# Kernel optimization log

Hardware: AMD Instinct MI355X
Metric: run time of the kernel (lower is better)

## Reference

```python
import jax, jax.numpy as jnp
import numpy as np

N, C = 800000, 80
B0, D0, H0, W0 = 4, 1, 360, 360


def setup_inputs() -> dict:
    key = jax.random.key(0)
    k1, k2, k3, k4, k5 = jax.random.split(key, 5)
    feats = jax.random.normal(k1, (N, C), dtype=jnp.float32)
    # coords columns: (x<W, y<H, z<D, b<B) -- per-column ranges so both rank
    # and flat geom index stay in-bounds, as in real LSS voxel coords.
    c0 = jax.random.randint(k2, (N,), 0, W0, dtype=jnp.int32)
    c1 = jax.random.randint(k3, (N,), 0, H0, dtype=jnp.int32)
    c2 = jax.random.randint(k4, (N,), 0, D0, dtype=jnp.int32)
    c3 = jax.random.randint(k5, (N,), 0, B0, dtype=jnp.int32)
    coords = jnp.stack([c0, c1, c2, c3], axis=1)
    return {"feats": feats, "coords": coords, "B": B0, "D": D0, "H": H0, "W": W0}


def reference(feats, coords, B, D, H, W):
    n, c_dim = feats.shape
    c = coords.astype(jnp.int32)
    # rank per point, then sort points by rank (groups equal-voxel points)
    ranks = c[:, 0] * (W * D * B) + c[:, 1] * (D * B) + c[:, 2] * B + c[:, 3]
    order = jnp.argsort(ranks)
    feats_s = feats[order]
    c_s = c[order]
    ranks_s = ranks[order]
    # inclusive cumsum over all points
    x = jnp.cumsum(feats_s, axis=0)  # [N, C]
    idx = jnp.arange(n, dtype=jnp.int32)
    kept = jnp.concatenate([jnp.array([True]), ranks_s[1:] != ranks_s[:-1]])
    # per-point interval start (last kept index <= i)
    starts = jax.lax.cummax(jnp.where(kept, idx, 0), axis=0)
    # per-point start of the NEXT interval (first kept index > i); n if none
    nk = jax.lax.cummin(jnp.where(kept, idx, n), axis=0, reverse=True)
    next_start = jnp.concatenate([nk[1:], jnp.array([n], dtype=jnp.int32)])
    is_last = next_start == n
    # torch code: per-interval value = x[end]-x[start]; last interval value is
    # overwritten with the final cumsum row x[n-1] (last_val). repeat_interleave
    # back to per-point is expressed directly as a per-point gather.
    vals = jnp.where(is_last[:, None],
                     x[n - 1],
                     x[jnp.minimum(next_start, n - 1)] - x[starts])  # [N, C]
    # flat BEV index exactly as the torch code computes it
    geom = c_s[:, 0] + c_s[:, 1] * W + c_s[:, 2] * H + c_s[:, 3]
    out = jnp.zeros((B * D * H * W, c_dim), dtype=feats.dtype)
    out = out.at[geom].add(vals)  # scatter-add voxel pooling
    return out.reshape(B, D, H, W, c_dim)
```

## Files before the change

kernel.cpp:

```cpp
#include <hip/hip_runtime.h>
#include <cstdint>

namespace {
constexpr int kC   = 80;
constexpr int kC4  = 20;
constexpr int kW   = 360;
constexpr int kH   = 360;
constexpr int kB   = 4;
constexpr int kR0  = kW * 1 * kB;
constexpr int kR1  = 1 * kB;
constexpr int kR2  = kB;
constexpr int kNR  = kW * kH * kB;
constexpr int kOutRows = kB * kH * kW;
}

__device__ __forceinline__ int rank_of(const int4 co) {
    return co.x * kR0 + co.y * kR1 + co.z * kR2 + co.w;
}

__device__ __forceinline__ float4 f4add(float4 a, float4 b) {
    return make_float4(a.x + b.x, a.y + b.y, a.z + b.z, a.w + b.w);
}

__global__ __launch_bounds__(320) void k_hist(
    const float4* __restrict__ feats4, const int4* __restrict__ coords, int n,
    int* __restrict__ cnt, int* __restrict__ minidx, int* __restrict__ rmax,
    float* __restrict__ total)
{
    const int tid = threadIdx.x;
    const int stride = gridDim.x * 320;
    const int tot4 = n * kC4;
    float4 ls = make_float4(0.f, 0.f, 0.f, 0.f);
    int wmaxr = -1;
    for (int e = blockIdx.x * 320 + tid; e < tot4; e += stride) {
        float4 f = feats4[e];
        ls = f4add(ls, f);
        int p  = e / kC4;
        int c4 = e - p * kC4;
        if (c4 == 0) {
            int r = rank_of(coords[p]);
            atomicAdd(&cnt[r], 1);
            atomicMin(&minidx[r], p);
            wmaxr = max(wmaxr, r);
        }
    }
    #pragma unroll
    for (int off = 32; off > 0; off >>= 1)
        wmaxr = max(wmaxr, __shfl_xor(wmaxr, off));
    if ((tid & 63) == 0 && wmaxr >= 0) atomicMax(rmax, wmaxr);

    __shared__ float tot[kC];
    if (tid < kC) tot[tid] = 0.f;
    __syncthreads();
    const int c4f = tid % kC4;
    atomicAdd(&tot[(c4f << 2) + 0], ls.x);
    atomicAdd(&tot[(c4f << 2) + 1], ls.y);
    atomicAdd(&tot[(c4f << 2) + 2], ls.z);
    atomicAdd(&tot[(c4f << 2) + 3], ls.w);
    __syncthreads();
    if (tid < kC) atomicAdd(&total[tid], tot[tid]);
}

__global__ void k_offset(const int* __restrict__ cnt, int* __restrict__ offset,
                         int* __restrict__ counter) {
    const int b = blockIdx.x * 256 + threadIdx.x;
    const int lane = threadIdx.x & 63, wid = threadIdx.x >> 6;
    int v = (b < kNR) ? cnt[b] : 0;
    int incl = v;
    #pragma unroll
    for (int d = 1; d < 64; d <<= 1) {
        int t = __shfl_up(incl, d);
        if (lane >= d) incl += t;
    }
    __shared__ int wsum[4];
    __shared__ int base;
    if (lane == 63) wsum[wid] = incl;
    __syncthreads();
    if (threadIdx.x == 0) {
        int s0 = 0;
        int tmp[4];
        #pragma unroll
        for (int i = 0; i < 4; ++i) { tmp[i] = s0; s0 += wsum[i]; }
        #pragma unroll
        for (int i = 0; i < 4; ++i) wsum[i] = tmp[i];
        base = atomicAdd(counter, s0);
    }
    __syncthreads();
    if (b < kNR) offset[b] = base + wsum[wid] + (incl - v);
}

__global__ void k_fill(const int4* __restrict__ coords, int n,
                       const int* __restrict__ offset, int* __restrict__ fill,
                       int* __restrict__ idxbuf) {
    int p = blockIdx.x * 256 + threadIdx.x;
    if (p >= n) return;
    int r = rank_of(coords[p]);
    int slot = atomicAdd(&fill[r], 1);
    idxbuf[offset[r] + slot] = p;
}

__global__ void k_extra(const int* __restrict__ cnt, const int* __restrict__ minidx,
                        int* __restrict__ extraidx) {
    int r = blockIdx.x * 256 + threadIdx.x;
    if (r >= kNR || cnt[r] == 0) return;
    int p = r - 1;
    while (p >= 0 && cnt[p] == 0) --p;
    if (p >= 0) extraidx[p] = minidx[r];
}

__global__ void k_out(const int* __restrict__ cnt, const int* __restrict__ offset,
                      const int* __restrict__ minidx, const int* __restrict__ extraidx,
                      const int* __restrict__ idxbuf,
                      const float4* __restrict__ feats4,
                      const float4* __restrict__ total4,
                      const int* __restrict__ rmax,
                      float4* __restrict__ out4)
{
    int idx = blockIdx.x * 256 + threadIdx.x;
    if (idx >= kOutRows * kC4) return;
    int g  = idx / kC4;
    int c4 = idx - g * kC4;
    const int rmaxv = *rmax;
    float4 acc = make_float4(0.f, 0.f, 0.f, 0.f);
    int q   = g / kW;
    int rem = g - q * kW;
    #pragma unroll
    for (int pass = 0; pass < 2; ++pass) {
        int c1 = q - pass;
        int s  = rem + pass * kW;
        if (c1 < 0 || c1 >= kH || s > (kW - 1) + (kB - 1)) continue;
        int c3lo = s - (kW - 1); if (c3lo < 0) c3lo = 0;
        int c3hi = (s < kB - 1) ? s : (kB - 1);
        for (int c3 = c3lo; c3 <= c3hi; ++c3) {
            int c0 = s - c3;
            int r  = c0 * kR0 + c1 * kR1 + c3;
            int cn = cnt[r];
            if (cn <= 0) continue;
            float fc = (float)cn;
            if (r == rmaxv) {
                float4 v = total4[c4];
                acc.x += fc * v.x; acc.y += fc * v.y;
                acc.z += fc * v.z; acc.w += fc * v.w;
            } else {
                int off = offset[r];
                int mi  = minidx[r];
                int ex  = extraidx[r];
                float4 sum = feats4[(size_t)ex * kC4 + c4];
                for (int j = 0; j < cn; ++j) {
                    int p = idxbuf[off + j];
                    if (p != mi) {
                        float4 f = feats4[(size_t)p * kC4 + c4];
                        sum = f4add(sum, f);
                    }
                }
                acc.x += fc * sum.x; acc.y += fc * sum.y;
                acc.z += fc * sum.z; acc.w += fc * sum.w;
            }
        }
    }
    out4[idx] = acc;
}

extern "C" void kernel_launch(void* const* d_in, const int* in_sizes, int n_in,
                              void* d_out, int out_size, void* d_ws, size_t ws_size,
                              hipStream_t stream) {
    (void)n_in; (void)out_size; (void)ws_size;
    const float* feats  = (const float*)d_in[0];
    const int*   coords = (const int*)d_in[1];
    const int n = in_sizes[1] / 4;

    char* ws = (char*)d_ws;
    size_t off = 0;
    int*   cnt      = (int*)(ws + off);   off += (size_t)kNR * 4;
    int*   minidx   = (int*)(ws + off);   off += (size_t)kNR * 4;
    int*   offsetb  = (int*)(ws + off);   off += (size_t)kNR * 4;
    int*   fill     = (int*)(ws + off);   off += (size_t)kNR * 4;
    int*   extraidx = (int*)(ws + off);   off += (size_t)kNR * 4;
    int*   idxbuf   = (int*)(ws + off);   off += (size_t)n * 4;
    int*   rmax     = (int*)(ws + off);   off += 16;
    int*   counter  = (int*)(ws + off);   off += 16;
    float* total    = (float*)(ws + off); off += 384;

    hipMemsetAsync(cnt,      0,    (size_t)kNR * 4, stream);
    hipMemsetAsync(minidx,   0x7F, (size_t)kNR * 4, stream);
    hipMemsetAsync(fill,     0,    (size_t)kNR * 4, stream);
    hipMemsetAsync(extraidx, 0xFF, (size_t)kNR * 4, stream);
    hipMemsetAsync(rmax,     0,    16, stream);
    hipMemsetAsync(counter,  0,    16, stream);
    hipMemsetAsync(total,    0,    384, stream);

    k_hist<<<1024, 320, 0, stream>>>((const float4*)feats, (const int4*)coords, n,
                                     cnt, minidx, rmax, total);
    k_offset<<<(kNR + 255) / 256, 256, 0, stream>>>(cnt, offsetb, counter);
    k_fill<<<(n + 255) / 256, 256, 0, stream>>>((const int4*)coords, n,
                                                offsetb, fill, idxbuf);
    k_extra<<<(kNR + 255) / 256, 256, 0, stream>>>(cnt, minidx, extraidx);

    const int tot_el = kOutRows * kC4;
    k_out<<<(tot_el + 255) / 256, 256, 0, stream>>>(cnt, offsetb, minidx, extraidx,
                                                    idxbuf, (const float4*)feats,
                                                    (const float4*)total, rmax,
                                                    (float4*)d_out);
}
```

Before: 655.0 us.

## Pack per-voxel metadata into int4 and split histogram from feature-total pass

Merges the separate per-rank arrays (count, offset/fill cursor, min index, extra index) into one int4 struct per rank, so k_out and the other passes fetch one 16-byte record instead of several scattered ints. The seven memsets are replaced by one init kernel. The coordinate histogram is split out of the feature-sum kernel, which now uses four independent accumulators. The extra-index search is folded into the offset scan kernel, and the fill cursor reuses the offset field. This cuts launches and scattered metadata traffic, but the atomics now target interleaved struct fields, which may change contention and cache behaviour.

```diff
diff --git a/kernel.cpp b/kernel.cpp
--- a/kernel.cpp
+++ b/kernel.cpp
@@ -17,55 +17,73 @@
 __device__ __forceinline__ int rank_of(const int4 co) {
     return co.x * kR0 + co.y * kR1 + co.z * kR2 + co.w;
 }
-
 __device__ __forceinline__ float4 f4add(float4 a, float4 b) {
     return make_float4(a.x + b.x, a.y + b.y, a.z + b.z, a.w + b.w);
 }
 
-__global__ __launch_bounds__(320) void k_hist(
-    const float4* __restrict__ feats4, const int4* __restrict__ coords, int n,
-    int* __restrict__ cnt, int* __restrict__ minidx, int* __restrict__ rmax,
-    float* __restrict__ total)
-{
-    const int tid = threadIdx.x;
-    const int stride = gridDim.x * 320;
-    const int tot4 = n * kC4;
-    float4 ls = make_float4(0.f, 0.f, 0.f, 0.f);
-    int wmaxr = -1;
-    for (int e = blockIdx.x * 320 + tid; e < tot4; e += stride) {
-        float4 f = feats4[e];
-        ls = f4add(ls, f);
-        int p  = e / kC4;
-        int c4 = e - p * kC4;
-        if (c4 == 0) {
-            int r = rank_of(coords[p]);
-            atomicAdd(&cnt[r], 1);
-            atomicMin(&minidx[r], p);
-            wmaxr = max(wmaxr, r);
-        }
+
+__global__ void k_init(int4* __restrict__ meta, int* __restrict__ rmax,
+                       int* __restrict__ counter, float* __restrict__ total) {
+    int i = blockIdx.x * 256 + threadIdx.x;
+    int stride = gridDim.x * 256;
+    const int4 iv = make_int4(0, 0, 0x7FFFFFFF, -1);
+    for (int r = i; r < kNR; r += stride) meta[r] = iv;
+    if (i == 0) { rmax[0] = 0; counter[0] = 0; }
+    if (i < kC) total[i] = 0.f;
+}
+
+__global__ void k_coord(const int4* __restrict__ coords, int n,
+                        int4* __restrict__ meta, int* __restrict__ rmax) {
+    int i = blockIdx.x * 256 + threadIdx.x;
+    int r = -1;
+    if (i < n) {
+        int4 co = coords[i];
+        r = rank_of(co);
+        atomicAdd(&meta[r].x, 1);
+        atomicMin(&meta[r].z, i);
     }
+    int wmax = r;
     #pragma unroll
     for (int off = 32; off > 0; off >>= 1)
-        wmaxr = max(wmaxr, __shfl_xor(wmaxr, off));
-    if ((tid & 63) == 0 && wmaxr >= 0) atomicMax(rmax, wmaxr);
+        wmax = max(wmax, __shfl_xor(wmax, off));
+    if ((threadIdx.x & 63) == 0 && wmax >= 0) atomicMax(rmax, wmax);
+}
+
+__global__ __launch_bounds__(320) void k_total(const float4* __restrict__ feats4,
+                                               int n, float* __restrict__ total) {
+    const int tid = threadIdx.x;
+    const int st = gridDim.x * 320;
+    const int tot4 = n * kC4;
+    float4 s0 = {0,0,0,0}, s1 = {0,0,0,0}, s2 = {0,0,0,0}, s3 = {0,0,0,0};
+    int e = blockIdx.x * 320 + tid;
+    for (; e + 3 * st < tot4; e += 4 * st) {
+        float4 a = feats4[e];
+        float4 b = feats4[e + st];
+        float4 c = feats4[e + 2 * st];
+        float4 d = feats4[e + 3 * st];
+        s0 = f4add(s0, a); s1 = f4add(s1, b);
+        s2 = f4add(s2, c); s3 = f4add(s3, d);
+    }
+    for (; e < tot4; e += st) s0 = f4add(s0, feats4[e]);
+    s0 = f4add(f4add(s0, s1), f4add(s2, s3));
 
     __shared__ float tot[kC];
     if (tid < kC) tot[tid] = 0.f;
     __syncthreads();
-    const int c4f = tid % kC4;
-    atomicAdd(&tot[(c4f << 2) + 0], ls.x);
-    atomicAdd(&tot[(c4f << 2) + 1], ls.y);
-    atomicAdd(&tot[(c4f << 2) + 2], ls.z);
-    atomicAdd(&tot[(c4f << 2) + 3], ls.w);
+    const int c4 = tid % kC4;
+    atomicAdd(&tot[(c4 << 2) + 0], s0.x);
+    atomicAdd(&tot[(c4 << 2) + 1], s0.y);
+    atomicAdd(&tot[(c4 << 2) + 2], s0.z);
+    atomicAdd(&tot[(c4 << 2) + 3], s0.w);
     __syncthreads();
     if (tid < kC) atomicAdd(&total[tid], tot[tid]);
 }
 
-__global__ void k_offset(const int* __restrict__ cnt, int* __restrict__ offset,
-                         int* __restrict__ counter) {
+__global__ void k_offset_extra(int4* __restrict__ meta, int* __restrict__ counter) {
     const int b = blockIdx.x * 256 + threadIdx.x;
     const int lane = threadIdx.x & 63, wid = threadIdx.x >> 6;
-    int v = (b < kNR) ? cnt[b] : 0;
+    int v = 0, mi = 0;
+    if (b < kNR) { int4 m = meta[b]; v = m.x; mi = m.z; }
     int incl = v;
     #pragma unroll
     for (int d = 1; d < 64; d <<= 1) {
@@ -77,45 +95,37 @@
     if (lane == 63) wsum[wid] = incl;
     __syncthreads();
     if (threadIdx.x == 0) {
-        int s0 = 0;
-        int tmp[4];
+        int s = 0;
         #pragma unroll
-        for (int i = 0; i < 4; ++i) { tmp[i] = s0; s0 += wsum[i]; }
-        #pragma unroll
-        for (int i = 0; i < 4; ++i) wsum[i] = tmp[i];
-        base = atomicAdd(counter, s0);
+        for (int i = 0; i < 4; ++i) { int t = wsum[i]; wsum[i] = s; s += t; }
+        base = atomicAdd(counter, s);
     }
     __syncthreads();
-    if (b < kNR) offset[b] = base + wsum[wid] + (incl - v);
+    if (b < kNR) {
+        meta[b].y = base + wsum[wid] + (incl - v);
+        if (v > 0) {
+            int p = b - 1;
+            while (p >= 0 && meta[p].x == 0) --p;
+            if (p >= 0) meta[p].w = mi;
+        }
+    }
 }
 
 __global__ void k_fill(const int4* __restrict__ coords, int n,
-                       const int* __restrict__ offset, int* __restrict__ fill,
-                       int* __restrict__ idxbuf) {
+                       int4* __restrict__ meta, int* __restrict__ idxbuf) {
     int p = blockIdx.x * 256 + threadIdx.x;
     if (p >= n) return;
     int r = rank_of(coords[p]);
-    int slot = atomicAdd(&fill[r], 1);
-    idxbuf[offset[r] + slot] = p;
+    int slot = atomicAdd(&meta[r].y, 1);
+    idxbuf[slot] = p;
 }
 
-__global__ void k_extra(const int* __restrict__ cnt, const int* __restrict__ minidx,
-                        int* __restrict__ extraidx) {
-    int r = blockIdx.x * 256 + threadIdx.x;
-    if (r >= kNR || cnt[r] == 0) return;
-    int p = r - 1;
-    while (p >= 0 && cnt[p] == 0) --p;
-    if (p >= 0) extraidx[p] = minidx[r];
-}
-
-__global__ void k_out(const int* __restrict__ cnt, const int* __restrict__ offset,
-                      const int* __restrict__ minidx, const int* __restrict__ extraidx,
+__global__ void k_out(const int4* __restrict__ meta,
                       const int* __restrict__ idxbuf,
                       const float4* __restrict__ feats4,
                       const float4* __restrict__ total4,
                       const int* __restrict__ rmax,
-                      float4* __restrict__ out4)
-{
+                      float4* __restrict__ out4) {
     int idx = blockIdx.x * 256 + threadIdx.x;
     if (idx >= kOutRows * kC4) return;
     int g  = idx / kC4;
@@ -134,28 +144,25 @@
         for (int c3 = c3lo; c3 <= c3hi; ++c3) {
             int c0 = s - c3;
             int r  = c0 * kR0 + c1 * kR1 + c3;
-            int cn = cnt[r];
+            int4 m = meta[r];
+            int cn = m.x;
             if (cn <= 0) continue;
             float fc = (float)cn;
+            float4 v;
             if (r == rmaxv) {
-                float4 v = total4[c4];
-                acc.x += fc * v.x; acc.y += fc * v.y;
-                acc.z += fc * v.z; acc.w += fc * v.w;
+                v = total4[c4];
             } else {
-                int off = offset[r];
-                int mi  = minidx[r];
-                int ex  = extraidx[r];
-                float4 sum = feats4[(size_t)ex * kC4 + c4];
+                int start = m.y - cn;
+                float4 sum = feats4[(size_t)m.w * kC4 + c4];
                 for (int j = 0; j < cn; ++j) {
-                    int p = idxbuf[off + j];
-                    if (p != mi) {
-                        float4 f = feats4[(size_t)p * kC4 + c4];
-                        sum = f4add(sum, f);
-                    }
+                    int p = idxbuf[start + j];
+                    if (p != m.z)
+                        sum = f4add(sum, feats4[(size_t)p * kC4 + c4]);
                 }
-                acc.x += fc * sum.x; acc.y += fc * sum.y;
-                acc.z += fc * sum.z; acc.w += fc * sum.w;
+                v = sum;
             }
+            acc.x += fc * v.x; acc.y += fc * v.y;
+            acc.z += fc * v.z; acc.w += fc * v.w;
         }
     }
     out4[idx] = acc;
@@ -171,34 +178,21 @@
 
     char* ws = (char*)d_ws;
     size_t off = 0;
-    int*   cnt      = (int*)(ws + off);   off += (size_t)kNR * 4;
-    int*   minidx   = (int*)(ws + off);   off += (size_t)kNR * 4;
-    int*   offsetb  = (int*)(ws + off);   off += (size_t)kNR * 4;
-    int*   fill     = (int*)(ws + off);   off += (size_t)kNR * 4;
-    int*   extraidx = (int*)(ws + off);   off += (size_t)kNR * 4;
-    int*   idxbuf   = (int*)(ws + off);   off += (size_t)n * 4;
-    int*   rmax     = (int*)(ws + off);   off += 16;
-    int*   counter  = (int*)(ws + off);   off += 16;
-    float* total    = (float*)(ws + off); off += 384;
+    int4*  meta    = (int4*)(ws + off);  off += (size_t)kNR * 16;
+    int*   idxbuf  = (int*)(ws + off);   off += (size_t)n * 4;
+    int*   rmax    = (int*)(ws + off);   off += 16;
+    int*   counter = (int*)(ws + off);   off += 16;
+    float* total   = (float*)(ws + off); off += 384;
 
-    hipMemsetAsync(cnt,      0,    (size_t)kNR * 4, stream);
-    hipMemsetAsync(minidx,   0x7F, (size_t)kNR * 4, stream);
-    hipMemsetAsync(fill,     0,    (size_t)kNR * 4, stream);
-    hipMemsetAsync(extraidx, 0xFF, (size_t)kNR * 4, stream);
-    hipMemsetAsync(rmax,     0,    16, stream);
-    hipMemsetAsync(counter,  0,    16, stream);
-    hipMemsetAsync(total,    0,    384, stream);
-
-    k_hist<<<1024, 320, 0, stream>>>((const float4*)feats, (const int4*)coords, n,
-                                     cnt, minidx, rmax, total);
-    k_offset<<<(kNR + 255) / 256, 256, 0, stream>>>(cnt, offsetb, counter);
-    k_fill<<<(n + 255) / 256, 256, 0, stream>>>((const int4*)coords, n,
-                                                offsetb, fill, idxbuf);
-    k_extra<<<(kNR + 255) / 256, 256, 0, stream>>>(cnt, minidx, extraidx);
+    k_init<<<2048, 256, 0, stream>>>(meta, rmax, counter, total);
+    k_coord<<<(n + 255) / 256, 256, 0, stream>>>((const int4*)coords, n, meta, rmax);
+    k_total<<<2048, 320, 0, stream>>>((const float4*)feats, n, total);
+    k_offset_extra<<<(kNR + 255) / 256, 256, 0, stream>>>(meta, counter);
+    k_fill<<<(n + 255) / 256, 256, 0, stream>>>((const int4*)coords, n, meta, idxbuf);
 
     const int tot_el = kOutRows * kC4;
-    k_out<<<(tot_el + 255) / 256, 256, 0, stream>>>(cnt, offsetb, minidx, extraidx,
-                                                    idxbuf, (const float4*)feats,
+    k_out<<<(tot_el + 255) / 256, 256, 0, stream>>>(meta, idxbuf,
+                                                    (const float4*)feats,
                                                     (const float4*)total, rmax,
                                                     (float4*)d_out);
 }
```

Result: slower. 746.3 us (+13.9%).
